# Kernel optimization log

Measured on AMD Instinct MI355X. Metric: run time of the kernel, lower is better.

## Reference

```python
import jax, jax.numpy as jnp
import numpy as np

BATCH = 32768
NJETS = 10
NCOMBOS = 22
FF = 200
NSEL = 6
EPS = 1e-5
METRIC = jnp.array([1.0, -1.0, -1.0, -1.0], dtype=jnp.float32)  # (E,px,py,pz) Minkowski


def _cola(v, w_combo):
    # v: [b, n, 4]; w_combo: [c, n] -> [b, n+c, 4] (identity rows + learned combos)
    combos = jnp.einsum('cj,bjv->bcv', w_combo, v)
    return jnp.concatenate([v, combos], axis=1)


def _lola(v, w_e, w_d):
    # v: [b, n, 4] -> [b, n, 5] features: m2, pT, E, w_e.E, w_d.d2
    m2 = jnp.einsum('biv,v,biv->bi', v, METRIC, v)           # invariant mass^2
    pt = jnp.sqrt(v[..., 1] ** 2 + v[..., 2] ** 2)           # transverse momentum
    E = v[..., 0]
    we = jnp.einsum('ij,bj->bi', w_e, E)
    # pairwise Minkowski distances via gram trick (avoids [b,n,n,4] tensor)
    gram = jnp.einsum('biv,v,bjv->bij', v, METRIC, v)        # [b, n, n]
    d2 = m2[:, :, None] + m2[:, None, :] - 2.0 * gram
    wd = jnp.einsum('ij,bij->bi', w_d, d2)
    return jnp.stack([m2, pt, E, we, wd], axis=-1)


def _batchnorm(x, gamma, beta):
    # torch BatchNorm1d in train mode: per-feature batch mean / biased var
    mu = jnp.mean(x, axis=0)
    var = jnp.mean((x - mu) ** 2, axis=0)
    return (x - mu) * jax.lax.rsqrt(var + EPS) * gamma + beta


def _head(v, cola_w, w_e, w_d, bn_g, bn_b, w1, b1, w2, b2):
    x = _cola(v, cola_w)
    f = _lola(x, w_e, w_d).reshape(x.shape[0], -1)  # [b, ntotal*5]
    f = _batchnorm(f, bn_g, bn_b)
    h = jax.nn.relu(f @ w1.T + b1)
    return h @ w2.T + b2


def setup_inputs() -> dict:
    key = jax.random.key(0)
    ks = jax.random.split(key, 20)
    n_isr = NJETS + NCOMBOS   # 32
    n_dec = NSEL + NCOMBOS    # 28
    f_isr, f_dec = n_isr * 5, n_dec * 5
    rn = lambda k, s, sc=0.1: jax.random.normal(k, s, jnp.float32) * sc
    return {
        'vectors': jax.random.normal(ks[0], (BATCH, NJETS, 4), jnp.float32),
        'isr_cola_w': rn(ks[1], (NCOMBOS, NJETS)),
        'isr_we': rn(ks[2], (n_isr, n_isr)),
        'isr_wd': rn(ks[3], (n_isr, n_isr)),
        'isr_bn_g': jnp.ones((f_isr,), jnp.float32),
        'isr_bn_b': jnp.zeros((f_isr,), jnp.float32),
        'isr_w1': rn(ks[4], (FF, f_isr)),
        'isr_b1': jnp.zeros((FF,), jnp.float32),
        'isr_w2': rn(ks[5], (NJETS, FF)),
        'isr_b2': jnp.zeros((NJETS,), jnp.float32),
        'dec_cola_w': rn(ks[6], (NCOMBOS, NSEL)),
        'dec_we': rn(ks[7], (n_dec, n_dec)),
        'dec_wd': rn(ks[8], (n_dec, n_dec)),
        'dec_bn_g': jnp.ones((f_dec,), jnp.float32),
        'dec_bn_b': jnp.zeros((f_dec,), jnp.float32),
        'dec_w1': rn(ks[9], (FF, f_dec)),
        'dec_b1': jnp.zeros((FF,), jnp.float32),
        'dec_w2': rn(ks[10], (11, FF)),
        'dec_b2': jnp.zeros((11,), jnp.float32),
    }


def reference(vectors, isr_cola_w, isr_we, isr_wd, isr_bn_g, isr_bn_b,
              isr_w1, isr_b1, isr_w2, isr_b2,
              dec_cola_w, dec_we, dec_wd, dec_bn_g, dec_bn_b,
              dec_w1, dec_b1, dec_w2, dec_b2):
    out_isr = _head(vectors, isr_cola_w, isr_we, isr_wd, isr_bn_g, isr_bn_b,
                    isr_w1, isr_b1, isr_w2, isr_b2)  # [b, njets]
    # iterative argmin+delete of (njets-6) jets == keep top-6 scores, original order
    scores = jax.lax.stop_gradient(out_isr)  # torch code detaches isrtag
    _, idx = jax.lax.top_k(scores, NSEL)
    idx = jnp.sort(idx, axis=1)  # np.delete preserves original ordering
    selected = jnp.take_along_axis(vectors, idx[:, :, None], axis=1)  # [b, 6, 4]
    out_dec = _head(selected, dec_cola_w, dec_we, dec_wd, dec_bn_g, dec_bn_b,
                    dec_w1, dec_b1, dec_w2, dec_b2)  # [b, 11]
    return jnp.concatenate([out_isr, out_dec], axis=1)  # [b, njets+11]
```

## Files before the change

kernel.cpp:

```cpp
#include <hip/hip_runtime.h>


#define BATCH 32768
#define NJ 10
#define FFDIM 200
#define OUTSTRIDE 21
#define NFEATBLK 4096

typedef float v2f __attribute__((ext_vector_type(2)));

template<int NIN, int NP>
__global__ __launch_bounds__(256) void feat_kernel(
    const float* __restrict__ vin,
    const float* __restrict__ cola,
    const float* __restrict__ we,
    const float* __restrict__ wd,
    float* __restrict__ fout,
    float* __restrict__ psum,
    float* __restrict__ psq)
{
    constexpr int NC = 22;
    constexpr int F  = NP * 5;
    constexpr int RB = 8;
    constexpr int SW = NP + 1;
    constexpr int SF = F + 8;
    __shared__ float s_cola[NC * NIN];
    __shared__ float s_we[NP * SW];
    __shared__ float s_wd[NP * SW];
    __shared__ float4 s_x[RB][NP];
    __shared__ float s_m2[RB][NP];
    __shared__ float s_f[RB * SF];

    const int tid = threadIdx.x;
    const int blk = blockIdx.x;

    for (int k = tid; k < NC * NIN; k += 256) s_cola[k] = cola[k];
    for (int k = tid; k < NP * NP; k += 256) {
        const int i2 = k / NP, j2 = k - i2 * NP;
        s_we[i2 * SW + j2] = we[k];
        s_wd[i2 * SW + j2] = wd[k];
    }
    for (int k = tid; k < RB * NIN * 4; k += 256)
        ((float*)&s_x[0][0])[(k / (NIN * 4)) * NP * 4 + (k % (NIN * 4))] =
            vin[(size_t)blk * RB * NIN * 4 + k];
    __syncthreads();

    const int r = tid >> 5;
    const int i = tid & 31;

    if (i >= NIN && i < NP) {
        const int c = i - NIN;
        float4 x = make_float4(0.f, 0.f, 0.f, 0.f);
        #pragma unroll
        for (int j = 0; j < NIN; j++) {
            const float w = s_cola[c * NIN + j];
            const float4 xj = s_x[r][j];
            x.x += w * xj.x; x.y += w * xj.y; x.z += w * xj.z; x.w += w * xj.w;
        }
        s_x[r][i] = x;
    }
    __syncthreads();

    float m2 = 0.f, pt = 0.f;
    float4 xi = make_float4(0.f, 0.f, 0.f, 0.f);
    if (i < NP) {
        xi = s_x[r][i];
        m2 = xi.x * xi.x - xi.y * xi.y - xi.z * xi.z - xi.w * xi.w;
        pt = sqrtf(xi.y * xi.y + xi.z * xi.z);
        s_m2[r][i] = m2;
    }
    __syncthreads();
    if (i < NP) {
        float wesum = 0.f, wdsum = 0.f;
        for (int j = 0; j < NP; j++) {
            const float4 xj = s_x[r][j];
            wesum += s_we[i * SW + j] * xj.x;
            const float g = xi.x * xj.x - xi.y * xj.y - xi.z * xj.z - xi.w * xj.w;
            wdsum += s_wd[i * SW + j] * (m2 + s_m2[r][j] - 2.0f * g);
        }
        s_f[r * SF + i * 5 + 0] = m2;
        s_f[r * SF + i * 5 + 1] = pt;
        s_f[r * SF + i * 5 + 2] = xi.x;
        s_f[r * SF + i * 5 + 3] = wesum;
        s_f[r * SF + i * 5 + 4] = wdsum;
    }
    __syncthreads();

    const size_t base = (size_t)(blk >> 2) * F * 32 + (blk & 3) * 8;
    for (int q = tid; q < F * RB; q += 256) {
        const int c = q >> 3, rr = q & 7;
        fout[base + (size_t)c * 32 + rr] = s_f[rr * SF + c];
    }

    if (tid < F) {
        float s = 0.f, s2 = 0.f;
        #pragma unroll
        for (int rr = 0; rr < RB; rr++) {
            const float v = s_f[rr * SF + tid];
            s += v; s2 += v * v;
        }
        psum[(size_t)tid * NFEATBLK + blk] = s;
        psq [(size_t)tid * NFEATBLK + blk] = s2;
    }
}

template<int F>
__global__ __launch_bounds__(256) void bn_reduce(
    const float* __restrict__ psum, const float* __restrict__ psq,
    const float* __restrict__ gamma, const float* __restrict__ beta,
    float* __restrict__ bn)
{
    __shared__ float s1[256], s2[256];
    const int f = blockIdx.x, tid = threadIdx.x;
    float a = 0.f, b = 0.f;
    for (int bk = tid; bk < NFEATBLK; bk += 256) {
        a += psum[(size_t)f * NFEATBLK + bk];
        b += psq [(size_t)f * NFEATBLK + bk];
    }
    s1[tid] = a; s2[tid] = b; __syncthreads();
    for (int s = 128; s > 0; s >>= 1) {
        if (tid < s) { s1[tid] += s1[tid + s]; s2[tid] += s2[tid + s]; }
        __syncthreads();
    }
    if (tid == 0) {
        const float mu  = s1[0] / (float)BATCH;
        const float var = s2[0] / (float)BATCH - mu * mu;
        const float sc  = gamma[f] * rsqrtf(var + 1e-5f);
        bn[f]     = sc;
        bn[F + f] = beta[f] - mu * sc;
    }
}

template<int NF, int NOUT, bool SELECT>
__global__ __launch_bounds__(256, 4) void mlp_kernel(
    const float* __restrict__ fin,
    const float* __restrict__ bn,
    const float* __restrict__ w1,
    const float* __restrict__ b1,
    const float* __restrict__ w2,
    const float* __restrict__ b2,
    const float* __restrict__ vectors,
    float* __restrict__ selout,
    float* __restrict__ out,
    int out_off)
{
    constexpr int RB = 32;
    constexpr int RP = 36;
    __shared__ __align__(16) float U[FFDIM * RP];
    __shared__ float s_scale[NF], s_shift[NF];
    __shared__ float s_out[RB * 12];
    __shared__ int   s_idx[RB * 6];

    const int tid = threadIdx.x;
    const int blk = blockIdx.x;

    for (int k = tid; k < NF; k += 256) { s_scale[k] = bn[k]; s_shift[k] = bn[NF + k]; }
    __syncthreads();

    {
        const float4* fb4 = reinterpret_cast<const float4*>(fin + (size_t)blk * NF * 32);
        for (int q4 = tid; q4 < NF * 8; q4 += 256) {
            const int c = q4 >> 3, r4a = (q4 & 7) * 4;
            const float4 v = fb4[q4];
            const float sc = s_scale[c], sh = s_shift[c];
            float4 o;
            o.x = v.x * sc + sh; o.y = v.y * sc + sh;
            o.z = v.z * sc + sh; o.w = v.w * sc + sh;
            *reinterpret_cast<float4*>(&U[c * RP + r4a]) = o;
        }
    }
    __syncthreads();

    const int r4 = (tid & 7) * 4;
    const int nc = tid >> 3;
    const int n6ok = (nc < FFDIM - 192);

    const float* wrow[7];
    float bb[7];
    #pragma unroll
    for (int j = 0; j < 6; j++) {
        wrow[j] = w1 + (size_t)(nc + 32 * j) * NF;
        bb[j] = b1[nc + 32 * j];
    }
    wrow[6] = w1 + (size_t)(n6ok ? (nc + 192) : nc) * NF;
    bb[6] = n6ok ? b1[nc + 192] : 0.f;

    v2f acc[7][2];
    #pragma unroll
    for (int j = 0; j < 7; j++) { acc[j][0] = (v2f){0.f, 0.f}; acc[j][1] = (v2f){0.f, 0.f}; }

    constexpr int NF4 = NF / 4;
    float4 wcur[7], wnxt[7];
    #pragma unroll
    for (int j = 0; j < 7; j++)
        wcur[j] = *reinterpret_cast<const float4*>(wrow[j]);

    for (int kc = 0; kc < NF4; kc++) {
        const int k = kc * 4;
        const int kn = (kc + 1 < NF4) ? (k + 4) : k;
        #pragma unroll
        for (int j = 0; j < 7; j++)
            wnxt[j] = *reinterpret_cast<const float4*>(wrow[j] + kn);

        const float4 f0 = *reinterpret_cast<const float4*>(&U[(k + 0) * RP + r4]);
        const float4 f1 = *reinterpret_cast<const float4*>(&U[(k + 1) * RP + r4]);
        const float4 f2 = *reinterpret_cast<const float4*>(&U[(k + 2) * RP + r4]);
        const float4 f3 = *reinterpret_cast<const float4*>(&U[(k + 3) * RP + r4]);
        const v2f f0l = (v2f){f0.x, f0.y}, f0h = (v2f){f0.z, f0.w};
        const v2f f1l = (v2f){f1.x, f1.y}, f1h = (v2f){f1.z, f1.w};
        const v2f f2l = (v2f){f2.x, f2.y}, f2h = (v2f){f2.z, f2.w};
        const v2f f3l = (v2f){f3.x, f3.y}, f3h = (v2f){f3.z, f3.w};

        #pragma unroll
        for (int j = 0; j < 7; j++) {
            const v2f wx = (v2f){wcur[j].x, wcur[j].x};
            const v2f wy = (v2f){wcur[j].y, wcur[j].y};
            const v2f wz = (v2f){wcur[j].z, wcur[j].z};
            const v2f ww = (v2f){wcur[j].w, wcur[j].w};
            acc[j][0] += wx * f0l; acc[j][0] += wy * f1l;
            acc[j][0] += wz * f2l; acc[j][0] += ww * f3l;
            acc[j][1] += wx * f0h; acc[j][1] += wy * f1h;
            acc[j][1] += wz * f2h; acc[j][1] += ww * f3h;
        }
        #pragma unroll
        for (int j = 0; j < 7; j++) wcur[j] = wnxt[j];
    }
    __syncthreads();

    #pragma unroll
    for (int j = 0; j < 7; j++) {
        if (j < 6 || n6ok) {
            const int n = nc + 32 * j;
            float4 h;
            h.x = acc[j][0][0] + bb[j]; h.x = h.x > 0.f ? h.x : 0.f;
            h.y = acc[j][0][1] + bb[j]; h.y = h.y > 0.f ? h.y : 0.f;
            h.z = acc[j][1][0] + bb[j]; h.z = h.z > 0.f ? h.z : 0.f;
            h.w = acc[j][1][1] + bb[j]; h.w = h.w > 0.f ? h.w : 0.f;
            *reinterpret_cast<float4*>(&U[n * RP + r4]) = h;
        }
    }
    __syncthreads();

    {
        const int r = tid & 31, og = tid >> 5;
        for (int o = og; o < NOUT; o += 8) {
            v2f a2 = (v2f){b2[o], 0.f};
            const v2f* w2p = reinterpret_cast<const v2f*>(w2 + (size_t)o * FFDIM);
            for (int kp = 0; kp < FFDIM / 2; kp++) {
                const v2f hh = (v2f){U[(2 * kp) * RP + r], U[(2 * kp + 1) * RP + r]};
                a2 += w2p[kp] * hh;
            }
            s_out[r * 12 + o] = a2[0] + a2[1];
        }
    }
    __syncthreads();

    if (SELECT) {
        if (tid < RB) {
            float sc[10];
            #pragma unroll
            for (int o = 0; o < 10; o++) sc[o] = s_out[tid * 12 + o];
            bool used[10];
            #pragma unroll
            for (int o = 0; o < 10; o++) used[o] = false;
            int ids[6];
            for (int k = 0; k < 6; k++) {
                float m = -3.0e38f; int mi = 0;
                for (int o = 0; o < 10; o++)
                    if (!used[o] && sc[o] > m) { m = sc[o]; mi = o; }
                used[mi] = true; ids[k] = mi;
            }
            for (int a2i = 1; a2i < 6; a2i++) {
                const int v = ids[a2i]; int bp = a2i - 1;
                while (bp >= 0 && ids[bp] > v) { ids[bp + 1] = ids[bp]; bp--; }
                ids[bp + 1] = v;
            }
            #pragma unroll
            for (int k = 0; k < 6; k++) s_idx[tid * 6 + k] = ids[k];
        }
        __syncthreads();
        for (int q = tid; q < RB * 6; q += 256) {
            const int r2 = q / 6, j = q - r2 * 6;
            reinterpret_cast<float4*>(selout)[(size_t)blk * RB * 6 + q] =
                reinterpret_cast<const float4*>(vectors)
                    [(size_t)(blk * RB + r2) * NJ + s_idx[r2 * 6 + j]];
        }
    }

    for (int q = tid; q < RB * NOUT; q += 256) {
        const int r2 = q / NOUT, o = q - r2 * NOUT;
        out[(size_t)(blk * RB + r2) * OUTSTRIDE + out_off + o] = s_out[r2 * 12 + o];
    }
}

extern "C" void kernel_launch(void* const* d_in, const int* in_sizes, int n_in,
                              void* d_out, int out_size, void* d_ws, size_t ws_size,
                              hipStream_t stream) {
    const float* vectors  = (const float*)d_in[0];
    const float* isr_cola = (const float*)d_in[1];
    const float* isr_we   = (const float*)d_in[2];
    const float* isr_wd   = (const float*)d_in[3];
    const float* isr_bn_g = (const float*)d_in[4];
    const float* isr_bn_b = (const float*)d_in[5];
    const float* isr_w1   = (const float*)d_in[6];
    const float* isr_b1   = (const float*)d_in[7];
    const float* isr_w2   = (const float*)d_in[8];
    const float* isr_b2   = (const float*)d_in[9];
    const float* dec_cola = (const float*)d_in[10];
    const float* dec_we   = (const float*)d_in[11];
    const float* dec_wd   = (const float*)d_in[12];
    const float* dec_bn_g = (const float*)d_in[13];
    const float* dec_bn_b = (const float*)d_in[14];
    const float* dec_w1   = (const float*)d_in[15];
    const float* dec_b1   = (const float*)d_in[16];
    const float* dec_w2   = (const float*)d_in[17];
    const float* dec_b2   = (const float*)d_in[18];
    float* out = (float*)d_out;
    float* ws  = (float*)d_ws;

    float* f_buf  = ws;
    float* sel    = f_buf + 5242880;
    float* ps     = sel + 786432;
    float* pq     = ps + 655360;
    float* bn_i   = pq + 655360;
    float* bn_d   = bn_i + 320;

    feat_kernel<10, 32><<<4096, 256, 0, stream>>>(vectors, isr_cola, isr_we, isr_wd,
                                                  f_buf, ps, pq);
    bn_reduce<160><<<160, 256, 0, stream>>>(ps, pq, isr_bn_g, isr_bn_b, bn_i);
    mlp_kernel<160, 10, true><<<1024, 256, 0, stream>>>(f_buf, bn_i, isr_w1, isr_b1,
                                                        isr_w2, isr_b2, vectors, sel,
                                                        out, 0);
    feat_kernel<6, 28><<<4096, 256, 0, stream>>>(sel, dec_cola, dec_we, dec_wd,
                                                 f_buf, ps, pq);
    bn_reduce<140><<<140, 256, 0, stream>>>(ps, pq, dec_bn_g, dec_bn_b, bn_d);
    mlp_kernel<140, 11, false><<<1024, 256, 0, stream>>>(f_buf, bn_d, dec_w1, dec_b1,
                                                         dec_w2, dec_b2, nullptr, nullptr,
                                                         out, 10);
}
```

Baseline: 173.8 us.

## Stage W1 k-slices through double-buffered shared memory in MLP kernel

Instead of each thread loading seven W1 rows straight from global memory (each weight row read by 8 threads), threads 0-199 cooperatively load one float4 k-slice per row into a double-buffered shared tile, prefetching the next slice in registers. Every thread then reads its seven weight vectors from LDS. This removes redundant global/L1 traffic for the weights, at the cost of a __syncthreads per k-step of 4 and extra LDS reads.

```diff
diff --git a/kernel.cpp b/kernel.cpp
--- a/kernel.cpp
+++ b/kernel.cpp
@@ -146,7 +146,9 @@
 {
     constexpr int RB = 32;
     constexpr int RP = 36;
+    constexpr int NF4 = NF / 4;
     __shared__ __align__(16) float U[FFDIM * RP];
+    __shared__ __align__(16) float s_w[2][224 * 4];
     __shared__ float s_scale[NF], s_shift[NF];
     __shared__ float s_out[RB * 12];
     __shared__ int   s_idx[RB * 6];
@@ -169,63 +171,56 @@
             *reinterpret_cast<float4*>(&U[c * RP + r4a]) = o;
         }
     }
-    __syncthreads();
-
-    const int r4 = (tid & 7) * 4;
+
+    const int rp = (tid & 7) * 4;
     const int nc = tid >> 3;
-    const int n6ok = (nc < FFDIM - 192);
-
-    const float* wrow[7];
+    const bool n6ok = (nc < FFDIM - 192);
+
     float bb[7];
     #pragma unroll
-    for (int j = 0; j < 6; j++) {
-        wrow[j] = w1 + (size_t)(nc + 32 * j) * NF;
-        bb[j] = b1[nc + 32 * j];
-    }
-    wrow[6] = w1 + (size_t)(n6ok ? (nc + 192) : nc) * NF;
+    for (int j = 0; j < 6; j++) bb[j] = b1[nc + 32 * j];
     bb[6] = n6ok ? b1[nc + 192] : 0.f;
 
     v2f acc[7][2];
     #pragma unroll
     for (int j = 0; j < 7; j++) { acc[j][0] = (v2f){0.f, 0.f}; acc[j][1] = (v2f){0.f, 0.f}; }
 
-    constexpr int NF4 = NF / 4;
-    float4 wcur[7], wnxt[7];
-    #pragma unroll
-    for (int j = 0; j < 7; j++)
-        wcur[j] = *reinterpret_cast<const float4*>(wrow[j]);
-
-    for (int kc = 0; kc < NF4; kc++) {
-        const int k = kc * 4;
-        const int kn = (kc + 1 < NF4) ? (k + 4) : k;
+    const bool wld = (tid < FFDIM);
+    float4 wv0, wv1;
+    if (wld) {
+        wv0 = *reinterpret_cast<const float4*>(w1 + (size_t)tid * NF);
+        wv1 = *reinterpret_cast<const float4*>(w1 + (size_t)tid * NF + 4);
+        *reinterpret_cast<float4*>(&s_w[0][tid * 4]) = wv0;
+    }
+    __syncthreads();
+
+    for (int kt = 0; kt < NF4; kt++) {
+        const int b = kt & 1;
+        float4 wq[7];
         #pragma unroll
         for (int j = 0; j < 7; j++)
-            wnxt[j] = *reinterpret_cast<const float4*>(wrow[j] + kn);
-
-        const float4 f0 = *reinterpret_cast<const float4*>(&U[(k + 0) * RP + r4]);
-        const float4 f1 = *reinterpret_cast<const float4*>(&U[(k + 1) * RP + r4]);
-        const float4 f2 = *reinterpret_cast<const float4*>(&U[(k + 2) * RP + r4]);
-        const float4 f3 = *reinterpret_cast<const float4*>(&U[(k + 3) * RP + r4]);
-        const v2f f0l = (v2f){f0.x, f0.y}, f0h = (v2f){f0.z, f0.w};
-        const v2f f1l = (v2f){f1.x, f1.y}, f1h = (v2f){f1.z, f1.w};
-        const v2f f2l = (v2f){f2.x, f2.y}, f2h = (v2f){f2.z, f2.w};
-        const v2f f3l = (v2f){f3.x, f3.y}, f3h = (v2f){f3.z, f3.w};
-
+            wq[j] = *reinterpret_cast<const float4*>(&s_w[b][(nc + 32 * j) * 4]);
         #pragma unroll
-        for (int j = 0; j < 7; j++) {
-            const v2f wx = (v2f){wcur[j].x, wcur[j].x};
-            const v2f wy = (v2f){wcur[j].y, wcur[j].y};
-            const v2f wz = (v2f){wcur[j].z, wcur[j].z};
-            const v2f ww = (v2f){wcur[j].w, wcur[j].w};
-            acc[j][0] += wx * f0l; acc[j][0] += wy * f1l;
-            acc[j][0] += wz * f2l; acc[j][0] += ww * f3l;
-            acc[j][1] += wx * f0h; acc[j][1] += wy * f1h;
-            acc[j][1] += wz * f2h; acc[j][1] += ww * f3h;
-        }
-        #pragma unroll
-        for (int j = 0; j < 7; j++) wcur[j] = wnxt[j];
-    }
-    __syncthreads();
+        for (int kk = 0; kk < 4; kk++) {
+            const float4 fa = *reinterpret_cast<const float4*>(&U[(kt * 4 + kk) * RP + rp]);
+            const v2f flo = (v2f){fa.x, fa.y}, fhi = (v2f){fa.z, fa.w};
+            #pragma unroll
+            for (int j = 0; j < 7; j++) {
+                const float w = kk == 0 ? wq[j].x : kk == 1 ? wq[j].y
+                              : kk == 2 ? wq[j].z : wq[j].w;
+                const v2f ws = (v2f){w, w};
+                acc[j][0] += ws * flo;
+                acc[j][1] += ws * fhi;
+            }
+        }
+        if (wld && kt + 1 < NF4) {
+            *reinterpret_cast<float4*>(&s_w[b ^ 1][tid * 4]) = wv1;
+            wv1 = wv0;
+            const int knext = (kt + 2 < NF4) ? (kt + 2) * 4 : (NF4 - 1) * 4;
+            wv1 = *reinterpret_cast<const float4*>(w1 + (size_t)tid * NF + knext);
+        }
+        __syncthreads();
+    }
 
     #pragma unroll
     for (int j = 0; j < 7; j++) {
@@ -236,7 +231,7 @@
             h.y = acc[j][0][1] + bb[j]; h.y = h.y > 0.f ? h.y : 0.f;
             h.z = acc[j][1][0] + bb[j]; h.z = h.z > 0.f ? h.z : 0.f;
             h.w = acc[j][1][1] + bb[j]; h.w = h.w > 0.f ? h.w : 0.f;
-            *reinterpret_cast<float4*>(&U[n * RP + r4]) = h;
+            *reinterpret_cast<float4*>(&U[n * RP + rp]) = h;
         }
     }
     __syncthreads();
```

New measurement: 159.1 us. 1.09x faster.
